# Optimization experiments

Hardware: AMD Instinct MI355X
Metric: run time of the kernel (lower is better)

Reference implementation:

```python
import jax, jax.numpy as jnp
import numpy as np


def setup_inputs() -> dict:
    key = jax.random.key(0)
    k1, k2, k3, k4, k5 = jax.random.split(key, 5)
    B, S, E, U = 32, 2048, 1024, 1024
    last_hidden_state = jax.random.normal(k1, (B, S, E), dtype=jnp.float32)
    attention_mask = jax.random.randint(k2, (B, S), 0, 2, dtype=jnp.int32)
    # ensure at least one valid token per row to avoid all -inf softmax
    attention_mask = attention_mask.at[:, 0].set(1)
    W = jax.random.normal(k3, (U, E), dtype=jnp.float32) * (E ** -0.5)
    Umat = jax.random.normal(k4, (U, E), dtype=jnp.float32) * (E ** -0.5)
    v = jax.random.normal(k5, (1, U), dtype=jnp.float32) * (U ** -0.5)
    return {"last_hidden_state": last_hidden_state, "attention_mask": attention_mask,
            "W": W, "U": Umat, "v": v}


def reference(last_hidden_state, attention_mask, W, U, v):
    # last_hidden_state: [B,S,E]; W,U: [units,E]; v: [1,units]
    Q = jnp.einsum('bse,ue->bsu', last_hidden_state, W)
    K = jnp.einsum('bse,ue->bsu', last_hidden_state, U)
    H = jnp.tanh(Q + K)                                   # [B,S,units]
    E = jnp.einsum('bsu,ou->bso', H, v)                   # [B,S,1]
    neg_inf = jnp.array(-jnp.inf, dtype=E.dtype)
    E = jnp.where(attention_mask[:, :, None] == 0, neg_inf, E)
    alpha = jax.nn.softmax(E, axis=1)                     # softmax over seq dim
    return jnp.sum(alpha * last_hidden_state, axis=1)     # [B,E]
```

## Files before the change

### kernel.cpp

```cpp
#include <hip/hip_runtime.h>
#include <hip/hip_bf16.h>


typedef short bf16x8 __attribute__((ext_vector_type(8)));
typedef float f32x4  __attribute__((ext_vector_type(4)));
typedef unsigned short u16x8 __attribute__((ext_vector_type(8)));

static __device__ __forceinline__ unsigned short f2bf(float f) {
    unsigned int x = __float_as_uint(f);
    unsigned int r = x + 0x7FFFu + ((x >> 16) & 1u);
    return (unsigned short)(r >> 16);
}

static __device__ __forceinline__ float fast_tanh(float x) {
    float e = __builtin_amdgcn_exp2f(x * 2.885390082f);
    float r = __builtin_amdgcn_rcpf(e + 1.0f);
    return __builtin_fmaf(-2.0f, r, 1.0f);
}

__global__ __launch_bounds__(256)
void prep_kernel(const float* __restrict__ W, const float* __restrict__ U,
                 unsigned short* __restrict__ wsum,
                 float* __restrict__ score, float* __restrict__ alpha,
                 float* __restrict__ out) {
    int g = blockIdx.x * 256 + threadIdx.x;
    int i4 = g * 4;
    float4 w = *(const float4*)&W[i4];
    float4 u = *(const float4*)&U[i4];
    ushort4 h;
    h.x = f2bf(w.x + u.x); h.y = f2bf(w.y + u.y);
    h.z = f2bf(w.z + u.z); h.w = f2bf(w.w + u.w);
    *(ushort4*)&wsum[i4] = h;
    if (g < 65536) { score[g] = 0.0f; alpha[g] = 0.0f; }
    if (g < 32768) out[g] = 0.0f;
}

__global__ __launch_bounds__(256)
void index_kernel(const int* __restrict__ mask, unsigned short* __restrict__ ridx,
                  int* __restrict__ cnt) {
    int b = blockIdx.x, t = threadIdx.x;
    const int* mrow = mask + b * 2048;
    int m[8], c = 0;
#pragma unroll
    for (int j = 0; j < 8; ++j) { m[j] = mrow[t * 8 + j]; c += (m[j] != 0); }
    __shared__ int sc[256];
    sc[t] = c;
    __syncthreads();
    for (int off = 1; off < 256; off <<= 1) {
        int v = (t >= off) ? sc[t - off] : 0;
        __syncthreads();
        sc[t] += v;
        __syncthreads();
    }
    int base = sc[t] - c;
    unsigned short* rb = ridx + b * 2048;
#pragma unroll
    for (int j = 0; j < 8; ++j)
        if (m[j]) rb[base++] = (unsigned short)(t * 8 + j);
    if (t == 255) cnt[b] = sc[255];
}

__global__ __launch_bounds__(256)
void gather_convert(const float* __restrict__ lhs, const unsigned short* __restrict__ ridx,
                    const int* __restrict__ cnt, unsigned short* __restrict__ Ab) {
    int b = blockIdx.y;
    int c = cnt[b];
    int cpad = (c + 127) & ~127;
    int r = blockIdx.x * 4 + (threadIdx.x >> 6);
    int lt = threadIdx.x & 63;
    if (r >= cpad) return;
    unsigned short* dst = Ab + ((size_t)b * 2048 + r) * 1024 + lt * 16;
    if (r < c) {
        int s = ridx[b * 2048 + r];
        const float* src = lhs + ((size_t)b * 2048 + s) * 1024 + lt * 16;
        float4 a0 = *(const float4*)(src + 0);
        float4 a1 = *(const float4*)(src + 4);
        float4 a2 = *(const float4*)(src + 8);
        float4 a3 = *(const float4*)(src + 12);
        u16x8 h0, h1;
        h0[0] = f2bf(a0.x); h0[1] = f2bf(a0.y); h0[2] = f2bf(a0.z); h0[3] = f2bf(a0.w);
        h0[4] = f2bf(a1.x); h0[5] = f2bf(a1.y); h0[6] = f2bf(a1.z); h0[7] = f2bf(a1.w);
        h1[0] = f2bf(a2.x); h1[1] = f2bf(a2.y); h1[2] = f2bf(a2.z); h1[3] = f2bf(a2.w);
        h1[4] = f2bf(a3.x); h1[5] = f2bf(a3.y); h1[6] = f2bf(a3.z); h1[7] = f2bf(a3.w);
        *(u16x8*)(dst + 0) = h0;
        *(u16x8*)(dst + 8) = h1;
    } else {
        u16x8 z = (u16x8){0,0,0,0,0,0,0,0};
        *(u16x8*)(dst + 0) = z;
        *(u16x8*)(dst + 8) = z;
    }
}

__global__ __launch_bounds__(256)
void score_gemm_bf16(const unsigned short* __restrict__ Ab,
                     const unsigned short* __restrict__ Bw,
                     const float* __restrict__ v, const int* __restrict__ cnt,
                     float* __restrict__ score) {
    const int K = 1024;
    __shared__ __align__(16) unsigned short As[128 * 64];
    __shared__ __align__(16) unsigned short Bs[128 * 64];

    const int bid    = (int)blockIdx.x;
    const int group  = bid >> 6;
    const int mt     = (group << 3) + (bid & 7);
    const int nI     = (bid >> 3) & 7;
    const int b      = mt >> 4;
    const int lm0    = (mt & 15) << 7;
    const int c      = cnt[b];
    if (lm0 >= ((c + 127) & ~127)) return;
    const int m0     = (b << 11) + lm0;
    const int n0     = nI << 7;

    const int t    = threadIdx.x;
    const int lane = t & 63;
    const int wave = t >> 6;
    const int wm   = (wave & 1) * 64;
    const int wn   = (wave >> 1) * 64;
    const int ml   = lane & 15;
    const int q    = lane >> 4;
    const int xorv = ml & 7;

    f32x4 acc[4][4];
#pragma unroll
    for (int i = 0; i < 4; ++i)
#pragma unroll
        for (int j = 0; j < 4; ++j)
            acc[i][j] = (f32x4){0.f, 0.f, 0.f, 0.f};

    const unsigned short* gA[4];
    const unsigned short* gB[4];
    unsigned short* lA[4];
    unsigned short* lB[4];
#pragma unroll
    for (int p = 0; p < 4; ++p) {
        int l   = p * 256 + wave * 64 + lane;
        int row = l >> 3;
        int kc  = (l & 7) ^ (row & 7);
        gA[p] = Ab + (size_t)(m0 + row) * K + kc * 8;
        gB[p] = Bw + (size_t)(n0 + row) * K + kc * 8;
        lA[p] = &As[(p * 4 + wave) * 512];
        lB[p] = &Bs[(p * 4 + wave) * 512];
    }

    for (int kk = 0; kk < K; kk += 64) {
#pragma unroll
        for (int p = 0; p < 4; ++p) {
            __builtin_amdgcn_global_load_lds((const __attribute__((address_space(1))) unsigned int*)gA[p],
                                             (__attribute__((address_space(3))) unsigned int*)lA[p], 16, 0, 0);
            __builtin_amdgcn_global_load_lds((const __attribute__((address_space(1))) unsigned int*)gB[p],
                                             (__attribute__((address_space(3))) unsigned int*)lB[p], 16, 0, 0);
            gA[p] += 64; gB[p] += 64;
        }
        __syncthreads();

#pragma unroll
        for (int s = 0; s < 2; ++s) {
            const int koff = ((s * 4 + q) ^ xorv) * 8;
            bf16x8 af[4], bf[4];
#pragma unroll
            for (int i = 0; i < 4; ++i)
                af[i] = *(const bf16x8*)&As[(wm + i * 16 + ml) * 64 + koff];
#pragma unroll
            for (int j = 0; j < 4; ++j)
                bf[j] = *(const bf16x8*)&Bs[(wn + j * 16 + ml) * 64 + koff];
#pragma unroll
            for (int i = 0; i < 4; ++i)
#pragma unroll
                for (int j = 0; j < 4; ++j)
                    acc[i][j] = __builtin_amdgcn_mfma_f32_16x16x32_bf16(af[i], bf[j], acc[i][j], 0, 0, 0);
        }
        __syncthreads();
    }

    float vw[4];
#pragma unroll
    for (int j = 0; j < 4; ++j)
        vw[j] = v[n0 + wn + j * 16 + ml];

#pragma unroll
    for (int i = 0; i < 4; ++i) {
#pragma unroll
        for (int r = 0; r < 4; ++r) {
            float val = 0.f;
#pragma unroll
            for (int j = 0; j < 4; ++j)
                val += fast_tanh(acc[i][j][r]) * vw[j];
#pragma unroll
            for (int off = 8; off > 0; off >>= 1)
                val += __shfl_xor(val, off, 64);
            if (ml == 0)
                atomicAdd(&score[m0 + wm + i * 16 + q * 4 + r], val);
        }
    }
}

#define LDSS 40
__global__ __launch_bounds__(256)
void score_gemm_f32stage(const float* __restrict__ A, const unsigned short* __restrict__ Bw,
                         const float* __restrict__ v, float* __restrict__ score) {
    const int K = 1024;
    __shared__ __align__(16) unsigned short As[128][LDSS];
    __shared__ __align__(16) unsigned short Bs[128][LDSS];
    const int n0 = (int)blockIdx.x * 128;
    const int m0 = (int)blockIdx.y * 128;
    const int t = threadIdx.x, lane = t & 63, wave = t >> 6;
    const int wm = (wave & 1) * 64, wn = (wave >> 1) * 64;
    const int ml = lane & 15, q = lane >> 4;
    f32x4 acc[4][4];
#pragma unroll
    for (int i = 0; i < 4; ++i)
#pragma unroll
        for (int j = 0; j < 4; ++j) acc[i][j] = (f32x4){0.f,0.f,0.f,0.f};
    const int sr = t >> 3, sc = (t & 7) * 4;
    for (int kk = 0; kk < K; kk += 32) {
#pragma unroll
        for (int p = 0; p < 4; ++p) {
            int r = sr + p * 32;
            float4 va = *(const float4*)&A[(size_t)(m0 + r) * K + kk + sc];
            ushort4 h; h.x = f2bf(va.x); h.y = f2bf(va.y); h.z = f2bf(va.z); h.w = f2bf(va.w);
            *(ushort4*)&As[r][sc] = h;
            ushort4 vb = *(const ushort4*)&Bw[(size_t)(n0 + r) * K + kk + sc];
            *(ushort4*)&Bs[r][sc] = vb;
        }
        __syncthreads();
        bf16x8 af[4], bf[4];
#pragma unroll
        for (int i = 0; i < 4; ++i) af[i] = *(const bf16x8*)&As[wm + i * 16 + ml][q * 8];
#pragma unroll
        for (int j = 0; j < 4; ++j) bf[j] = *(const bf16x8*)&Bs[wn + j * 16 + ml][q * 8];
#pragma unroll
        for (int i = 0; i < 4; ++i)
#pragma unroll
            for (int j = 0; j < 4; ++j)
                acc[i][j] = __builtin_amdgcn_mfma_f32_16x16x32_bf16(af[i], bf[j], acc[i][j], 0, 0, 0);
        __syncthreads();
    }
    float vw[4];
#pragma unroll
    for (int j = 0; j < 4; ++j) vw[j] = v[n0 + wn + j * 16 + ml];
#pragma unroll
    for (int i = 0; i < 4; ++i)
#pragma unroll
        for (int r = 0; r < 4; ++r) {
            float val = 0.f;
#pragma unroll
            for (int j = 0; j < 4; ++j) val += fast_tanh(acc[i][j][r]) * vw[j];
#pragma unroll
            for (int off = 8; off > 0; off >>= 1) val += __shfl_xor(val, off, 64);
            if (ml == 0) atomicAdd(&score[m0 + wm + i * 16 + q * 4 + r], val);
        }
}

__global__ __launch_bounds__(256)
void softmax_compact(const float* __restrict__ score, const unsigned short* __restrict__ ridx,
                     const int* __restrict__ cnt, float* __restrict__ alpha) {
    int b = blockIdx.x, t = threadIdx.x;
    int c = cnt[b];
    __shared__ float red[8];
    float sc[8];
    float mx = -1e30f;
#pragma unroll
    for (int i = 0; i < 8; ++i) {
        int k = i * 256 + t;
        sc[i] = (k < c) ? score[b * 2048 + k] : -1e30f;
        mx = fmaxf(mx, sc[i]);
    }
#pragma unroll
    for (int off = 32; off > 0; off >>= 1)
        mx = fmaxf(mx, __shfl_xor(mx, off, 64));
    if ((t & 63) == 0) red[t >> 6] = mx;
    __syncthreads();
    mx = fmaxf(fmaxf(red[0], red[1]), fmaxf(red[2], red[3]));
    float e[8], sum = 0.f;
#pragma unroll
    for (int i = 0; i < 8; ++i) {
        int k = i * 256 + t;
        e[i] = (k < c) ? __expf(sc[i] - mx) : 0.f;
        sum += e[i];
    }
#pragma unroll
    for (int off = 32; off > 0; off >>= 1)
        sum += __shfl_xor(sum, off, 64);
    if ((t & 63) == 0) red[4 + (t >> 6)] = sum;
    __syncthreads();
    float inv = 1.0f / (red[4] + red[5] + red[6] + red[7]);
#pragma unroll
    for (int i = 0; i < 8; ++i) {
        int k = i * 256 + t;
        if (k < c) {
            int s = ridx[b * 2048 + k];
            alpha[b * 2048 + s] = e[i] * inv;
        }
    }
}

__global__ __launch_bounds__(256)
void softmax_kernel(const float* __restrict__ score, const int* __restrict__ mask,
                    float* __restrict__ alpha) {
    const int S = 2048;
    int b = blockIdx.x, t = threadIdx.x;
    __shared__ float red[8];
    float sc[8]; int vd[8];
    float mx = -1e30f;
#pragma unroll
    for (int i = 0; i < 8; ++i) {
        int s = i * 256 + t;
        vd[i] = mask[b * S + s];
        sc[i] = score[b * S + s];
        if (vd[i]) mx = fmaxf(mx, sc[i]);
    }
#pragma unroll
    for (int off = 32; off > 0; off >>= 1)
        mx = fmaxf(mx, __shfl_xor(mx, off, 64));
    if ((t & 63) == 0) red[t >> 6] = mx;
    __syncthreads();
    mx = fmaxf(fmaxf(red[0], red[1]), fmaxf(red[2], red[3]));
    float e[8]; float sum = 0.f;
#pragma unroll
    for (int i = 0; i < 8; ++i) {
        e[i] = vd[i] ? __expf(sc[i] - mx) : 0.f;
        sum += e[i];
    }
#pragma unroll
    for (int off = 32; off > 0; off >>= 1)
        sum += __shfl_xor(sum, off, 64);
    if ((t & 63) == 0) red[4 + (t >> 6)] = sum;
    __syncthreads();
    float inv = 1.0f / (red[4] + red[5] + red[6] + red[7]);
#pragma unroll
    for (int i = 0; i < 8; ++i)
        alpha[b * S + i * 256 + t] = e[i] * inv;
}

__global__ __launch_bounds__(256)
void wsum_partial(const float* __restrict__ lhs, const float* __restrict__ alpha,
                  float* __restrict__ part) {
    const int S = 2048, E = 1024;
    int b = blockIdx.x >> 6;
    int seg = blockIdx.x & 63;
    int t = threadIdx.x;
    int s0 = seg * 32;
    const float* base = lhs + ((size_t)b * S + s0) * E + t * 4;
    const float* ap = alpha + b * S + s0;
    float4 acc = {0.f, 0.f, 0.f, 0.f};
#pragma unroll 4
    for (int s = 0; s < 32; ++s) {
        float a = ap[s];
        if (a != 0.f) {
            float4 x = *(const float4*)(base + (size_t)s * E);
            acc.x += a * x.x; acc.y += a * x.y; acc.z += a * x.z; acc.w += a * x.w;
        }
    }
    *(float4*)(part + (size_t)blockIdx.x * E + t * 4) = acc;
}

__global__ __launch_bounds__(256)
void wsum_reduce(const float* __restrict__ part, float* __restrict__ out) {
    int b = blockIdx.x >> 2;
    int e = (blockIdx.x & 3) * 256 + threadIdx.x;
    const float* p = part + (size_t)b * 64 * 1024 + e;
    float sum = 0.f;
#pragma unroll
    for (int s = 0; s < 64; ++s)
        sum += p[(size_t)s * 1024];
    out[b * 1024 + e] = sum;
}

__global__ __launch_bounds__(256)
void wsum_kernel(const float* __restrict__ lhs, const float* __restrict__ alpha,
                 float* __restrict__ out) {
    const int S = 2048, E = 1024;
    int b = blockIdx.x >> 6;
    int seg = blockIdx.x & 63;
    int t = threadIdx.x;
    int s0 = seg * 32;
    const float* base = lhs + ((size_t)b * S + s0) * E + t * 4;
    const float* ap = alpha + b * S + s0;
    float4 acc = {0.f, 0.f, 0.f, 0.f};
#pragma unroll 4
    for (int s = 0; s < 32; ++s) {
        float a = ap[s];
        if (a != 0.f) {
            float4 x = *(const float4*)(base + (size_t)s * E);
            acc.x += a * x.x; acc.y += a * x.y; acc.z += a * x.z; acc.w += a * x.w;
        }
    }
    float* o = out + b * E + t * 4;
    atomicAdd(o + 0, acc.x);
    atomicAdd(o + 1, acc.y);
    atomicAdd(o + 2, acc.z);
    atomicAdd(o + 3, acc.w);
}

extern "C" void kernel_launch(void* const* d_in, const int* in_sizes, int n_in,
                              void* d_out, int out_size, void* d_ws, size_t ws_size,
                              hipStream_t stream) {
    const float* lhs  = (const float*)d_in[0];
    const int*   mask = (const int*)d_in[1];
    const float* W    = (const float*)d_in[2];
    const float* Um   = (const float*)d_in[3];
    const float* v    = (const float*)d_in[4];
    float* out = (float*)d_out;

    char* ws = (char*)d_ws;
    unsigned short* wsum  = (unsigned short*)ws;
    float* score          = (float*)(ws + 2048u * 1024u);
    float* alpha          = (float*)(ws + 2304u * 1024u);
    unsigned short* ridx  = (unsigned short*)(ws + 2560u * 1024u);
    int* cnt              = (int*)(ws + 2688u * 1024u);
    unsigned short* Ab    = (unsigned short*)(ws + 2816u * 1024u);
    float* part           = (float*)(ws + 2816u * 1024u + 131072u * 1024u);
    const size_t need = 2816ull * 1024ull + 131072ull * 1024ull + 8192ull * 1024ull;

    prep_kernel<<<1024, 256, 0, stream>>>(W, Um, wsum, score, alpha, out);
    if (ws_size >= need) {
        index_kernel<<<32, 256, 0, stream>>>(mask, ridx, cnt);
        dim3 gg(512, 32);
        gather_convert<<<gg, 256, 0, stream>>>(lhs, ridx, cnt, Ab);
        score_gemm_bf16<<<4096, 256, 0, stream>>>(Ab, wsum, v, cnt, score);
        softmax_compact<<<32, 256, 0, stream>>>(score, ridx, cnt, alpha);
        wsum_partial<<<2048, 256, 0, stream>>>(lhs, alpha, part);
        wsum_reduce<<<128, 256, 0, stream>>>(part, out);
    } else {
        dim3 g1(8, 512);
        score_gemm_f32stage<<<g1, 256, 0, stream>>>(lhs, wsum, v, score);
        softmax_kernel<<<32, 256, 0, stream>>>(score, mask, alpha);
        wsum_kernel<<<2048, 256, 0, stream>>>(lhs, alpha, out);
    }
}
```

Baseline: 521.6 us.

## Reuse compacted bf16 rows for weighted sum and fuse prep with index kernel

The final weighted sum now reads the already-gathered, compacted bf16 copy of the valid rows instead of the full fp32 hidden state. Softmax writes alpha in compacted order, and the partial-sum plus reduce kernels are replaced by one kernel that accumulates with atomics. The prep and mask-index kernels are merged into a single launch. This cuts the bytes read for the weighted sum and removes two launches. In exchange, the weighted sum uses bf16 inputs, which lowers accuracy, and it runs with fewer blocks doing a longer sequential loop, so less memory traffic may be in flight.

```diff
diff --git a/kernel.cpp b/kernel.cpp
--- a/kernel.cpp
+++ b/kernel.cpp
@@ -19,45 +19,45 @@
 }
 
 __global__ __launch_bounds__(256)
-void prep_kernel(const float* __restrict__ W, const float* __restrict__ U,
-                 unsigned short* __restrict__ wsum,
-                 float* __restrict__ score, float* __restrict__ alpha,
-                 float* __restrict__ out) {
-    int g = blockIdx.x * 256 + threadIdx.x;
-    int i4 = g * 4;
-    float4 w = *(const float4*)&W[i4];
-    float4 u = *(const float4*)&U[i4];
-    ushort4 h;
-    h.x = f2bf(w.x + u.x); h.y = f2bf(w.y + u.y);
-    h.z = f2bf(w.z + u.z); h.w = f2bf(w.w + u.w);
-    *(ushort4*)&wsum[i4] = h;
-    if (g < 65536) { score[g] = 0.0f; alpha[g] = 0.0f; }
-    if (g < 32768) out[g] = 0.0f;
-}
-
-__global__ __launch_bounds__(256)
-void index_kernel(const int* __restrict__ mask, unsigned short* __restrict__ ridx,
-                  int* __restrict__ cnt) {
-    int b = blockIdx.x, t = threadIdx.x;
-    const int* mrow = mask + b * 2048;
-    int m[8], c = 0;
-#pragma unroll
-    for (int j = 0; j < 8; ++j) { m[j] = mrow[t * 8 + j]; c += (m[j] != 0); }
+void prep_index(const float* __restrict__ W, const float* __restrict__ U,
+                const int* __restrict__ mask,
+                unsigned short* __restrict__ wsum,
+                float* __restrict__ score, float* __restrict__ out,
+                unsigned short* __restrict__ ridx, int* __restrict__ cnt) {
     __shared__ int sc[256];
-    sc[t] = c;
-    __syncthreads();
-    for (int off = 1; off < 256; off <<= 1) {
-        int v = (t >= off) ? sc[t - off] : 0;
+    int blk = blockIdx.x, t = threadIdx.x;
+    if (blk < 1024) {
+        int g = blk * 256 + t;
+        int i4 = g * 4;
+        float4 w = *(const float4*)&W[i4];
+        float4 u = *(const float4*)&U[i4];
+        ushort4 h;
+        h.x = f2bf(w.x + u.x); h.y = f2bf(w.y + u.y);
+        h.z = f2bf(w.z + u.z); h.w = f2bf(w.w + u.w);
+        *(ushort4*)&wsum[i4] = h;
+        if (g < 65536) score[g] = 0.0f;
+        if (g < 32768) out[g] = 0.0f;
+    } else {
+        int b = blk - 1024;
+        const int* mrow = mask + b * 2048;
+        int m[8], c = 0;
+#pragma unroll
+        for (int j = 0; j < 8; ++j) { m[j] = mrow[t * 8 + j]; c += (m[j] != 0); }
+        sc[t] = c;
         __syncthreads();
-        sc[t] += v;
-        __syncthreads();
-    }
-    int base = sc[t] - c;
-    unsigned short* rb = ridx + b * 2048;
-#pragma unroll
-    for (int j = 0; j < 8; ++j)
-        if (m[j]) rb[base++] = (unsigned short)(t * 8 + j);
-    if (t == 255) cnt[b] = sc[255];
+        for (int off = 1; off < 256; off <<= 1) {
+            int v = (t >= off) ? sc[t - off] : 0;
+            __syncthreads();
+            sc[t] += v;
+            __syncthreads();
+        }
+        int base = sc[t] - c;
+        unsigned short* rb = ridx + b * 2048;
+#pragma unroll
+        for (int j = 0; j < 8; ++j)
+            if (m[j]) rb[base++] = (unsigned short)(t * 8 + j);
+        if (t == 255) cnt[b] = sc[255];
+    }
 }
 
 __global__ __launch_bounds__(256)
@@ -194,6 +194,74 @@
     }
 }
 
+__global__ __launch_bounds__(256)
+void softmax_compact(const float* __restrict__ score, const int* __restrict__ cnt,
+                     float* __restrict__ alphac) {
+    int b = blockIdx.x, t = threadIdx.x;
+    int c = cnt[b];
+    __shared__ float red[8];
+    float sc[8];
+    float mx = -1e30f;
+#pragma unroll
+    for (int i = 0; i < 8; ++i) {
+        int k = i * 256 + t;
+        sc[i] = (k < c) ? score[b * 2048 + k] : -1e30f;
+        mx = fmaxf(mx, sc[i]);
+    }
+#pragma unroll
+    for (int off = 32; off > 0; off >>= 1)
+        mx = fmaxf(mx, __shfl_xor(mx, off, 64));
+    if ((t & 63) == 0) red[t >> 6] = mx;
+    __syncthreads();
+    mx = fmaxf(fmaxf(red[0], red[1]), fmaxf(red[2], red[3]));
+    float e[8], sum = 0.f;
+#pragma unroll
+    for (int i = 0; i < 8; ++i) {
+        int k = i * 256 + t;
+        e[i] = (k < c) ? __expf(sc[i] - mx) : 0.f;
+        sum += e[i];
+    }
+#pragma unroll
+    for (int off = 32; off > 0; off >>= 1)
+        sum += __shfl_xor(sum, off, 64);
+    if ((t & 63) == 0) red[4 + (t >> 6)] = sum;
+    __syncthreads();
+    float inv = 1.0f / (red[4] + red[5] + red[6] + red[7]);
+#pragma unroll
+    for (int i = 0; i < 8; ++i) {
+        int k = i * 256 + t;
+        if (k < c) alphac[b * 2048 + k] = e[i] * inv;
+    }
+}
+
+__global__ __launch_bounds__(256)
+void wsum_bf16(const unsigned short* __restrict__ Ab, const float* __restrict__ alphac,
+               const int* __restrict__ cnt, float* __restrict__ out) {
+    int b   = blockIdx.x >> 4;
+    int seg = blockIdx.x & 15;
+    int t   = threadIdx.x;
+    int c   = cnt[b];
+    int per = (c + 15) >> 4;
+    int s0  = seg * per;
+    int s1  = min(s0 + per, c);
+    const float* ap = alphac + b * 2048;
+    const unsigned short* base = Ab + (size_t)b * 2048 * 1024 + t * 4;
+    float a0 = 0.f, a1 = 0.f, a2 = 0.f, a3 = 0.f;
+    for (int s = s0; s < s1; ++s) {
+        float a = ap[s];
+        ushort4 h = *(const ushort4*)(base + (size_t)s * 1024);
+        a0 = __builtin_fmaf(a, __uint_as_float((unsigned)h.x << 16), a0);
+        a1 = __builtin_fmaf(a, __uint_as_float((unsigned)h.y << 16), a1);
+        a2 = __builtin_fmaf(a, __uint_as_float((unsigned)h.z << 16), a2);
+        a3 = __builtin_fmaf(a, __uint_as_float((unsigned)h.w << 16), a3);
+    }
+    float* o = out + b * 1024 + t * 4;
+    atomicAdd(o + 0, a0);
+    atomicAdd(o + 1, a1);
+    atomicAdd(o + 2, a2);
+    atomicAdd(o + 3, a3);
+}
+
 #define LDSS 40
 __global__ __launch_bounds__(256)
 void score_gemm_f32stage(const float* __restrict__ A, const unsigned short* __restrict__ Bw,
@@ -252,49 +320,6 @@
 }
 
 __global__ __launch_bounds__(256)
-void softmax_compact(const float* __restrict__ score, const unsigned short* __restrict__ ridx,
-                     const int* __restrict__ cnt, float* __restrict__ alpha) {
-    int b = blockIdx.x, t = threadIdx.x;
-    int c = cnt[b];
-    __shared__ float red[8];
-    float sc[8];
-    float mx = -1e30f;
-#pragma unroll
-    for (int i = 0; i < 8; ++i) {
-        int k = i * 256 + t;
-        sc[i] = (k < c) ? score[b * 2048 + k] : -1e30f;
-        mx = fmaxf(mx, sc[i]);
-    }
-#pragma unroll
-    for (int off = 32; off > 0; off >>= 1)
-        mx = fmaxf(mx, __shfl_xor(mx, off, 64));
-    if ((t & 63) == 0) red[t >> 6] = mx;
-    __syncthreads();
-    mx = fmaxf(fmaxf(red[0], red[1]), fmaxf(red[2], red[3]));
-    float e[8], sum = 0.f;
-#pragma unroll
-    for (int i = 0; i < 8; ++i) {
-        int k = i * 256 + t;
-        e[i] = (k < c) ? __expf(sc[i] - mx) : 0.f;
-        sum += e[i];
-    }
-#pragma unroll
-    for (int off = 32; off > 0; off >>= 1)
-        sum += __shfl_xor(sum, off, 64);
-    if ((t & 63) == 0) red[4 + (t >> 6)] = sum;
-    __syncthreads();
-    float inv = 1.0f / (red[4] + red[5] + red[6] + red[7]);
-#pragma unroll
-    for (int i = 0; i < 8; ++i) {
-        int k = i * 256 + t;
-        if (k < c) {
-            int s = ridx[b * 2048 + k];
-            alpha[b * 2048 + s] = e[i] * inv;
-        }
-    }
-}
-
-__global__ __launch_bounds__(256)
 void softmax_kernel(const float* __restrict__ score, const int* __restrict__ mask,
                     float* __restrict__ alpha) {
     const int S = 2048;
@@ -330,40 +355,6 @@
 #pragma unroll
     for (int i = 0; i < 8; ++i)
         alpha[b * S + i * 256 + t] = e[i] * inv;
-}
-
-__global__ __launch_bounds__(256)
-void wsum_partial(const float* __restrict__ lhs, const float* __restrict__ alpha,
-                  float* __restrict__ part) {
-    const int S = 2048, E = 1024;
-    int b = blockIdx.x >> 6;
-    int seg = blockIdx.x & 63;
-    int t = threadIdx.x;
-    int s0 = seg * 32;
-    const float* base = lhs + ((size_t)b * S + s0) * E + t * 4;
-    const float* ap = alpha + b * S + s0;
-    float4 acc = {0.f, 0.f, 0.f, 0.f};
-#pragma unroll 4
-    for (int s = 0; s < 32; ++s) {
-        float a = ap[s];
-        if (a != 0.f) {
-            float4 x = *(const float4*)(base + (size_t)s * E);
-            acc.x += a * x.x; acc.y += a * x.y; acc.z += a * x.z; acc.w += a * x.w;
-        }
-    }
-    *(float4*)(part + (size_t)blockIdx.x * E + t * 4) = acc;
-}
-
-__global__ __launch_bounds__(256)
-void wsum_reduce(const float* __restrict__ part, float* __restrict__ out) {
-    int b = blockIdx.x >> 2;
-    int e = (blockIdx.x & 3) * 256 + threadIdx.x;
-    const float* p = part + (size_t)b * 64 * 1024 + e;
-    float sum = 0.f;
-#pragma unroll
-    for (int s = 0; s < 64; ++s)
-        sum += p[(size_t)s * 1024];
-    out[b * 1024 + e] = sum;
 }
 
 __global__ __launch_bounds__(256)
@@ -405,26 +396,23 @@
     char* ws = (char*)d_ws;
     unsigned short* wsum  = (unsigned short*)ws;
     float* score          = (float*)(ws + 2048u * 1024u);
-    float* alpha          = (float*)(ws + 2304u * 1024u);
+    float* alphac         = (float*)(ws + 2304u * 1024u);
     unsigned short* ridx  = (unsigned short*)(ws + 2560u * 1024u);
     int* cnt              = (int*)(ws + 2688u * 1024u);
     unsigned short* Ab    = (unsigned short*)(ws + 2816u * 1024u);
-    float* part           = (float*)(ws + 2816u * 1024u + 131072u * 1024u);
-    const size_t need = 2816ull * 1024ull + 131072ull * 1024ull + 8192ull * 1024ull;
-
-    prep_kernel<<<1024, 256, 0, stream>>>(W, Um, wsum, score, alpha, out);
+    const size_t need = 2816ull * 1024ull + 131072ull * 1024ull;
+
+    prep_index<<<1056, 256, 0, stream>>>(W, Um, mask, wsum, score, out, ridx, cnt);
     if (ws_size >= need) {
-        index_kernel<<<32, 256, 0, stream>>>(mask, ridx, cnt);
         dim3 gg(512, 32);
         gather_convert<<<gg, 256, 0, stream>>>(lhs, ridx, cnt, Ab);
         score_gemm_bf16<<<4096, 256, 0, stream>>>(Ab, wsum, v, cnt, score);
-        softmax_compact<<<32, 256, 0, stream>>>(score, ridx, cnt, alpha);
-        wsum_partial<<<2048, 256, 0, stream>>>(lhs, alpha, part);
-        wsum_reduce<<<128, 256, 0, stream>>>(part, out);
+        softmax_compact<<<32, 256, 0, stream>>>(score, cnt, alphac);
+        wsum_bf16<<<512, 256, 0, stream>>>(Ab, alphac, cnt, out);
     } else {
         dim3 g1(8, 512);
         score_gemm_f32stage<<<g1, 256, 0, stream>>>(lhs, wsum, v, score);
-        softmax_kernel<<<32, 256, 0, stream>>>(score, mask, alpha);
-        wsum_kernel<<<2048, 256, 0, stream>>>(lhs, alpha, out);
-    }
-}
+        softmax_kernel<<<32, 256, 0, stream>>>(score, mask, alphac);
+        wsum_kernel<<<2048, 256, 0, stream>>>(lhs, alphac, out);
+    }
+}
```

Result: no change. 514.1 us (-1.4%).
